# Kernel optimization log

Measured on AMD Instinct MI355X. Metric: run time of the kernel, lower is better.

Reference implementation:

```python
import jax, jax.numpy as jnp
import numpy as np

NUM_CLASSES = 21
THRESH = 0.5
NEG_POS = 3
VAR0, VAR1 = 0.1, 0.2  # SSD cfg['variance']
B, P, O = 32, 32768, 50


def point_form(boxes):
    # center form (cx,cy,w,h) -> corner form (xmin,ymin,xmax,ymax)
    return jnp.concatenate([boxes[:, :2] - boxes[:, 2:] / 2,
                            boxes[:, :2] + boxes[:, 2:] / 2], axis=1)


def jaccard(box_a, box_b):
    # box_a [A,4], box_b [B,4], corner form -> IoU [A,B]
    max_xy = jnp.minimum(box_a[:, None, 2:], box_b[None, :, 2:])
    min_xy = jnp.maximum(box_a[:, None, :2], box_b[None, :, :2])
    inter = jnp.prod(jnp.clip(max_xy - min_xy, 0.0, None), axis=2)
    area_a = jnp.prod(box_a[:, 2:] - box_a[:, :2], axis=1)[:, None]
    area_b = jnp.prod(box_b[:, 2:] - box_b[:, :2], axis=1)[None, :]
    return inter / (area_a + area_b - inter)


def encode(matched, priors):
    # matched corner form [P,4], priors center form [P,4]
    g_cxcy = ((matched[:, :2] + matched[:, 2:]) / 2 - priors[:, :2]) / (VAR0 * priors[:, 2:])
    g_wh = jnp.log((matched[:, 2:] - matched[:, :2]) / priors[:, 2:]) / VAR1
    return jnp.concatenate([g_cxcy, g_wh], axis=1)


def match_one(truths, labels, priors):
    # truths [O,4] corner, labels [O], priors [P,4] center
    overlaps = jaccard(truths, point_form(priors))          # [O,P]
    best_prior_idx = jnp.argmax(overlaps, axis=1)           # [O]
    best_truth_overlap = jnp.max(overlaps, axis=0)          # [P]
    best_truth_idx = jnp.argmax(overlaps, axis=0)           # [P]
    # ensure every gt matches its best prior
    best_truth_overlap = best_truth_overlap.at[best_prior_idx].set(2.0)
    best_truth_idx = best_truth_idx.at[best_prior_idx].set(jnp.arange(truths.shape[0]))
    matches = truths[best_truth_idx]                        # [P,4]
    conf = (labels[best_truth_idx] + 1.0).astype(jnp.int32)
    conf = jnp.where(best_truth_overlap < THRESH, 0, conf)
    return encode(matches, priors), conf


def setup_inputs() -> dict:
    key = jax.random.key(0)
    k1, k2, k3, k4, k5, k6 = jax.random.split(key, 6)
    loc_data = jax.random.normal(k1, (B, P, 4), dtype=jnp.float32)
    conf_data = jax.random.normal(k2, (B, P, NUM_CLASSES), dtype=jnp.float32)
    # priors in center form: centers in (0,1), sizes in (0.02, 0.5)
    cxy = jax.random.uniform(k3, (P, 2), dtype=jnp.float32)
    wh = jax.random.uniform(k4, (P, 2), dtype=jnp.float32, minval=0.02, maxval=0.5)
    priors = jnp.concatenate([cxy, wh], axis=1)
    # targets: valid corner-form boxes + label
    pts = jax.random.uniform(k5, (B, O, 2, 2), dtype=jnp.float32)
    xymin = pts.min(axis=2)
    xymax = jnp.maximum(pts.max(axis=2), xymin + 0.01)
    labels = jax.random.randint(k6, (B, O), 0, NUM_CLASSES - 1).astype(jnp.float32)
    targets = jnp.concatenate([xymin, xymax, labels[..., None]], axis=-1)
    return {"loc_data": loc_data, "conf_data": conf_data, "priors": priors, "targets": targets}


def reference(loc_data, conf_data, priors, targets):
    truths = targets[..., :4]
    labels = targets[..., 4]
    loc_t, conf_t = jax.vmap(match_one, in_axes=(0, 0, None))(truths, labels, priors)
    loc_t = jax.lax.stop_gradient(loc_t)
    conf_t = jax.lax.stop_gradient(conf_t)

    pos = conf_t > 0                                         # [B,P]
    # localization: smooth-L1, summed over positives
    diff = loc_data - loc_t
    ad = jnp.abs(diff)
    sl1 = jnp.where(ad < 1.0, 0.5 * diff * diff, ad - 0.5)
    loss_l = jnp.sum(sl1 * pos[..., None].astype(sl1.dtype))

    # per-prior softmax CE (logsumexp - true logit)
    lse = jax.nn.logsumexp(conf_data, axis=-1)               # [B,P]
    true_logit = jnp.take_along_axis(conf_data, conf_t[..., None], axis=-1)[..., 0]
    ce = lse - true_logit                                    # [B,P]

    # hard negative mining: rank negatives by CE (pos zeroed out)
    ce_mine = jnp.where(pos, 0.0, ce)
    loss_idx = jnp.argsort(-ce_mine, axis=1)
    idx_rank = jnp.argsort(loss_idx, axis=1)
    num_pos = jnp.sum(pos, axis=1, keepdims=True)            # [B,1]
    num_neg = jnp.clip(NEG_POS * num_pos, None, pos.shape[1] - 1)
    neg = idx_rank < num_neg

    sel = pos | neg
    loss_c = jnp.sum(jnp.where(sel, ce, 0.0))

    N = jnp.sum(num_pos).astype(loss_l.dtype)
    return loss_l / N, loss_c / N
```

## Files before the change

kernel.cpp:

```cpp
#include <hip/hip_runtime.h>
#include <math.h>

#define BB 32
#define PP 32768
#define OO 50
#define NT 25
#define NC 21
#define MPT 4

#define WBINLO (104 << 7)
#define WBINS  2048

typedef unsigned long long u64;
typedef unsigned int u32;
typedef unsigned char u8;

static constexpr u32 FORCED_HI = 0x40000000u;
static constexpr u32 HALF_BITS = 0x3F000000u;

static constexpr size_t OFF_WHC   = 0;
static constexpr size_t OFF_WHS   = OFF_WHC  + 4ull*BB*WBINS;
static constexpr size_t OFF_KEYS  = OFF_WHS  + 4ull*BB*WBINS;
static constexpr size_t OFF_NPOS  = OFF_KEYS + 8ull*BB*OO;
static constexpr size_t OFF_DACC  = OFF_NPOS + 128;
static constexpr size_t OFF_KEY2  = ((OFF_DACC + 8ull*3*BB + 127) & ~127ull);
static constexpr size_t ZERO_BYTES = OFF_KEY2 + 8ull*BB*PP;

__global__ __launch_bounds__(256) void zero_kernel(ulonglong2* __restrict__ dst, size_t n16) {
    size_t i = (size_t)blockIdx.x * 256 + threadIdx.x;
    if (i < n16) dst[i] = make_ulonglong2(0ull, 0ull);
}

static __device__ __forceinline__ float fast_div(float a, float b) {
    return a * __builtin_amdgcn_rcpf(b);
}

__global__ __launch_bounds__(256) void match_kernel(
    const float* __restrict__ priors, const float* __restrict__ targets,
    u64* __restrict__ key2, u64* __restrict__ keys)
{
#pragma clang fp contract(off)
    const int b = blockIdx.y;
    const int obase = blockIdx.z * NT;
    const int tid = threadIdx.x;
    const int lane = tid & 63, wid = tid >> 6;
    const int wbase = blockIdx.x * (256 * MPT) + wid * (64 * MPT);

    __shared__ float tr[NT * 5];
    __shared__ u64 wkeys[4][NT];
    if (tid < NT * 5) tr[tid] = targets[(size_t)b * OO * 5 + obase * 5 + tid];
    __syncthreads();

    float px1[MPT], py1[MPT], px2[MPT], py2[MPT], area_p[MPT];
#pragma unroll
    for (int s = 0; s < MPT; ++s) {
        int p = wbase + s * 64 + lane;
        float4 pr = *(const float4*)(priors + (size_t)p * 4);
        px1[s] = pr.x - pr.z * 0.5f; py1[s] = pr.y - pr.w * 0.5f;
        px2[s] = pr.x + pr.z * 0.5f; py2[s] = pr.y + pr.w * 0.5f;
        area_p[s] = (px2[s] - px1[s]) * (py2[s] - py1[s]);
    }

    float bestv[MPT]; int besto[MPT];
#pragma unroll
    for (int s = 0; s < MPT; ++s) { bestv[s] = -1.0f; besto[s] = 0; }

    for (int o = 0; o < NT; ++o) {
        float tx1 = tr[o*5+0], ty1 = tr[o*5+1], tx2 = tr[o*5+2], ty2 = tr[o*5+3];
        float area_t = (tx2 - tx1) * (ty2 - ty1);
        float iou[MPT];
#pragma unroll
        for (int s = 0; s < MPT; ++s) {
            float ix1 = fmaxf(tx1, px1[s]), iy1 = fmaxf(ty1, py1[s]);
            float ix2 = fminf(tx2, px2[s]), iy2 = fminf(ty2, py2[s]);
            float dx = fmaxf(ix2 - ix1, 0.0f), dy = fmaxf(iy2 - iy1, 0.0f);
            float inter = dx * dy;
            iou[s] = fast_div(inter, (area_t + area_p[s]) - inter);
            if (iou[s] > bestv[s]) { bestv[s] = iou[s]; besto[s] = o; }
        }
        float mv = fmaxf(fmaxf(iou[0], iou[1]), fmaxf(iou[2], iou[3]));
        for (int m = 1; m < 64; m <<= 1)
            mv = fmaxf(mv, __shfl_xor(mv, m, 64));
        u64 b0 = __ballot(iou[0] == mv);
        u64 b1 = __ballot(iou[1] == mv);
        u64 b2 = __ballot(iou[2] == mv);
        u64 b3 = __ballot(iou[3] == mv);
        if (lane == 0) {
            int s, l;
            if      (b0) { s = 0; l = __ffsll(b0) - 1; }
            else if (b1) { s = 1; l = __ffsll(b1) - 1; }
            else if (b2) { s = 2; l = __ffsll(b2) - 1; }
            else if (b3) { s = 3; l = __ffsll(b3) - 1; }
            else         { s = 0; l = 0; }
            u32 wp = (u32)(wbase + s * 64 + l);
            wkeys[wid][o] = ((u64)__float_as_uint(mv) << 32) | (u64)(0xFFFFFFFFu - wp);
        }
    }
#pragma unroll
    for (int s = 0; s < MPT; ++s) {
        int p = wbase + s * 64 + lane;
        u64 key = ((u64)__float_as_uint(bestv[s]) << 32)
                | (u64)(u32)(49 - (obase + besto[s]));
        atomicMax(&key2[(size_t)b * PP + p], key);
    }
    __syncthreads();
    if (tid < NT) {
        u64 k0 = wkeys[0][tid];
        for (int w = 1; w < 4; ++w) { u64 kw = wkeys[w][tid]; if (kw > k0) k0 = kw; }
        atomicMax(&keys[b * OO + obase + tid], k0);
    }
}

__global__ void override_kernel(const u64* __restrict__ keys, u64* __restrict__ key2) {
    const int b = blockIdx.x;
    const int o = threadIdx.x;
    if (o < OO) {
        u32 p = 0xFFFFFFFFu - (u32)(keys[b * OO + o] & 0xFFFFFFFFull);
        atomicMax(&key2[(size_t)b * PP + p],
                  ((u64)FORCED_HI << 32) | (u64)(u32)(64 + o));
    }
}

static __device__ __forceinline__ u32 top16bits(float v) {
    u32 u = __float_as_uint(v);
    return (v > 0.0f) ? u : 0u;
}

#define EL(k) ((((k) & 3) == 0) ? v[(k) >> 2].x : \
               (((k) & 3) == 1) ? v[(k) >> 2].y : \
               (((k) & 3) == 2) ? v[(k) >> 2].z : v[(k) >> 2].w)

__global__ __launch_bounds__(256) void score_kernel(
    const float* __restrict__ loc, const float* __restrict__ conf,
    const float* __restrict__ priors, const float* __restrict__ targets,
    const u64* __restrict__ key2,
    int* __restrict__ npos, double* __restrict__ dacc,
    u32* __restrict__ whc, float* __restrict__ whs)
{
    const int b = blockIdx.y;
    const int tid = threadIdx.x;
    const int p = blockIdx.x * 1024 + tid * 4;
    __shared__ float tr[OO * 5];
    __shared__ __align__(16) u32 hh[WBINS];
    __shared__ __align__(16) float hs[WBINS];
    if (tid < OO * 5) tr[tid] = targets[(size_t)b * OO * 5 + tid];
#pragma unroll
    for (int j = 0; j < WBINS / 256; ++j) { hh[j * 256 + tid] = 0; hs[j * 256 + tid] = 0.0f; }
    __syncthreads();

    ulonglong2 k01 = *(const ulonglong2*)(key2 + (size_t)b * PP + p);
    ulonglong2 k23 = *(const ulonglong2*)(key2 + (size_t)b * PP + p + 2);
    const u64 kk[4] = {k01.x, k01.y, k23.x, k23.y};

    const float4* cp = (const float4*)(conf + ((size_t)b * PP + p) * NC);
    float4 v[21];
    float cev[4];
    double l_l = 0.0, pce = 0.0; int np_ = 0;

#pragma unroll
    for (int r = 0; r < 4; ++r) {
        const int jlo = (r == 0) ? 0 : ((21 * (r - 1) + 20) / 4 + 1);
        const int jhi = (21 * r + 20) / 4;
#pragma unroll
        for (int j = jlo; j <= jhi; ++j) v[j] = cp[j];

        const u32 hi = (u32)(kk[r] >> 32);
        const u32 lo = (u32)kk[r];
        const bool forced = lo >= 64u;
        const int o = forced ? (int)(lo - 64u) : (int)(49u - lo);
        const bool pos = forced || hi >= HALF_BITS;
        const int conft = pos ? (int)(tr[o * 5 + 4] + 1.0f) : 0;

        float m = -1e30f;
#pragma unroll
        for (int c = 0; c < NC; ++c) m = fmaxf(m, EL(21 * r + c));
        float s = 0.0f, tl = 0.0f;
#pragma unroll
        for (int c = 0; c < NC; ++c) {
            float xx = EL(21 * r + c);
            s += expf(xx - m);
            if (c == conft) tl = xx;
        }
        float ce = (m + logf(s)) - tl;
        cev[r] = pos ? 0.0f : ce;

        if (pos) {
            np_ += 1; pce += (double)ce;
            float mx1 = tr[o*5+0], my1 = tr[o*5+1], mx2 = tr[o*5+2], my2 = tr[o*5+3];
            float4 pr = *(const float4*)(priors + (size_t)(p + r) * 4);
            float lt0 = ((mx1 + mx2) * 0.5f - pr.x) / (0.1f * pr.z);
            float lt1 = ((my1 + my2) * 0.5f - pr.y) / (0.1f * pr.w);
            float lt2 = logf((mx2 - mx1) / pr.z) / 0.2f;
            float lt3 = logf((my2 - my1) / pr.w) / 0.2f;
            float4 l4 = *(const float4*)(loc + ((size_t)b * PP + p + r) * 4);
            float lpv[4] = {l4.x, l4.y, l4.z, l4.w};
            float lt[4] = {lt0, lt1, lt2, lt3};
#pragma unroll
            for (int i2 = 0; i2 < 4; ++i2) {
                float d = lpv[i2] - lt[i2];
                float ad = fabsf(d);
                l_l += (double)(ad < 1.0f ? 0.5f * d * d : ad - 0.5f);
            }
        }
    }

#pragma unroll
    for (int r = 0; r < 4; ++r) {
        u32 t16 = top16bits(cev[r]) >> 16;
        if (t16 != 0) {
            int widx = ((int)t16 - WBINLO) >> 1;
            widx = widx < 0 ? 0 : (widx > WBINS - 1 ? WBINS - 1 : widx);
            atomicAdd(&hh[widx], 1u);
            atomicAdd(&hs[widx], cev[r]);
        }
    }
    __syncthreads();
#pragma unroll
    for (int j = 0; j < WBINS / 256; ++j) {
        u32 c = hh[j * 256 + tid];
        if (c) {
            atomicAdd(&whc[(size_t)b * WBINS + j * 256 + tid], c);
            atomicAdd(&whs[(size_t)b * WBINS + j * 256 + tid], hs[j * 256 + tid]);
        }
    }
    __syncthreads();
    double* rl = (double*)hh;
    double* rc = (double*)hs;
    int*    rn = (int*)(hh + 1024);
    rl[tid] = l_l; rc[tid] = pce; rn[tid] = np_;
    __syncthreads();
    for (int s2 = 128; s2 > 0; s2 >>= 1) {
        if (tid < s2) { rl[tid] += rl[tid+s2]; rc[tid] += rc[tid+s2]; rn[tid] += rn[tid+s2]; }
        __syncthreads();
    }
    if (tid == 0) {
        atomicAdd(&dacc[b], rl[0]);
        atomicAdd(&dacc[BB + b], rc[0]);
        atomicAdd(&npos[b], rn[0]);
    }
}

__global__ __launch_bounds__(256) void selwin_kernel(
    const u32* __restrict__ whc, const float* __restrict__ whs,
    const int* __restrict__ npos, double* __restrict__ dacc)
{
    const int b = blockIdx.x, tid = threadIdx.x;
    const int lane = tid & 63, wid = tid >> 6;
    int k = npos[b] * 3; if (k > PP - 1) k = PP - 1;
    if (k <= 0) return;
    const u32* hc = whc + (size_t)b * WBINS;
    const float* hsg = whs + (size_t)b * WBINS;

    __shared__ u32 ccnt_[WBINS / 256]; __shared__ float csum_[WBINS / 256];
    __shared__ u32 ct[256]; __shared__ float fs[256];
    __shared__ int s_cT; __shared__ u32 s_aboveC; __shared__ float s_aboveS;
    __shared__ u32 sT;

    for (int c = wid; c < WBINS / 256; c += 4) {
        u32 cnt = 0; float sm = 0.0f;
#pragma unroll
        for (int q = 0; q < 4; ++q) {
            int idx = c * 256 + q * 64 + lane;
            cnt += hc[idx];
            sm  += hsg[idx];
        }
        for (int m = 1; m < 64; m <<= 1) {
            cnt += __shfl_xor(cnt, m, 64);
            sm  += __shfl_xor(sm, m, 64);
        }
        if (lane == 0) { ccnt_[c] = cnt; csum_[c] = sm; }
    }
    if (tid == 0) sT = 0;
    __syncthreads();
    if (tid == 0) {
        u32 cum = 0; float scum = 0.0f; int cT = -1; u32 aboveC = 0; float aboveS = 0.0f;
        for (int c = WBINS / 256 - 1; c >= 0; --c) {
            if (cum + ccnt_[c] >= (u32)k) { cT = c; aboveC = cum; aboveS = scum; break; }
            cum += ccnt_[c]; scum += csum_[c];
        }
        s_cT = cT; s_aboveC = aboveC; s_aboveS = aboveS;
        if (cT < 0) dacc[2 * BB + b] = (double)scum;
    }
    __syncthreads();
    const int cT = s_cT;
    if (cT < 0) return;
    const u32 aboveC = s_aboveC; const float aboveS = s_aboveS;

    const u32 myc = hc[cT * 256 + tid];
    const float mys = hsg[cT * 256 + tid];
    ct[tid] = myc; fs[tid] = mys;
    __syncthreads();
    for (int off = 1; off < 256; off <<= 1) {
        u32 a1 = (tid + off < 256) ? ct[tid + off] : 0;
        float a2 = (tid + off < 256) ? fs[tid + off] : 0.0f;
        __syncthreads();
        ct[tid] += a1; fs[tid] += a2;
        __syncthreads();
    }
    if (aboveC + ct[tid] >= (u32)k) atomicMax(&sT, (u32)tid);
    __syncthreads();
    const int T = (int)sT;
    if (tid == T) {
        u32 aboveBinC = aboveC + ((T < 255) ? ct[T + 1] : 0);
        float aboveBinS = aboveS + ((T < 255) ? fs[T + 1] : 0.0f);
        int k2 = k - (int)aboveBinC;
        double avg = (double)mys / (double)myc;
        dacc[2 * BB + b] = (double)aboveBinS + (double)k2 * avg;
    }
}

__global__ void finalize_kernel(const int* __restrict__ npos,
                                const double* __restrict__ dacc, float* __restrict__ out) {
    if (threadIdx.x == 0 && blockIdx.x == 0) {
        double N = 0.0, ll = 0.0, lc = 0.0;
        for (int b = 0; b < BB; ++b) {
            N += (double)npos[b];
            ll += dacc[b];
            lc += dacc[BB + b] + dacc[2 * BB + b];
        }
        out[0] = (float)(ll / N);
        out[1] = (float)(lc / N);
    }
}

extern "C" void kernel_launch(void* const* d_in, const int* in_sizes, int n_in,
                              void* d_out, int out_size, void* d_ws, size_t ws_size,
                              hipStream_t stream) {
    const float* loc     = (const float*)d_in[0];
    const float* conf    = (const float*)d_in[1];
    const float* priors  = (const float*)d_in[2];
    const float* targets = (const float*)d_in[3];
    char* ws = (char*)d_ws;
    u32*    whc   = (u32*)   (ws + OFF_WHC);
    float*  whs   = (float*) (ws + OFF_WHS);
    u64*    keys  = (u64*)   (ws + OFF_KEYS);
    int*    npos  = (int*)   (ws + OFF_NPOS);
    double* dacc  = (double*)(ws + OFF_DACC);
    u64*    key2  = (u64*)   (ws + OFF_KEY2);
    float*  out   = (float*)d_out;

    const size_t n16 = ZERO_BYTES / 16;
    zero_kernel<<<(unsigned)((n16 + 255) / 256), 256, 0, stream>>>((ulonglong2*)ws, n16);
    match_kernel<<<dim3(PP / (256 * MPT), BB, 2), 256, 0, stream>>>(priors, targets, key2, keys);
    override_kernel<<<BB, 64, 0, stream>>>(keys, key2);
    score_kernel<<<dim3(PP / 1024, BB), 256, 0, stream>>>(loc, conf, priors, targets, key2, npos, dacc, whc, whs);
    selwin_kernel<<<BB, 256, 0, stream>>>(whc, whs, npos, dacc);
    finalize_kernel<<<1, 64, 0, stream>>>(npos, dacc, out);
}
```

Measured before the change: 98.97 us.

## Replace per-prior atomicMax with split key buffers and fold forced override into scoring

Each match_kernel half now writes plain stores into its own key2 slice instead of doing atomicMax into a shared slice. The score kernel loads both halves and takes the max. The key2 region no longer needs zeroing, which removes about 8 MB of memset traffic. The override kernel is also removed: the score kernel loads each image's 50 forced-match prior indices into shared memory and checks every prior against them. This saves a launch and the atomics, at the cost of double key2 reads in scoring and a 50-iteration compare loop per thread.

```diff
diff --git a/kernel.cpp b/kernel.cpp
--- a/kernel.cpp
+++ b/kernel.cpp
@@ -15,7 +15,6 @@
 typedef unsigned int u32;
 typedef unsigned char u8;
 
-static constexpr u32 FORCED_HI = 0x40000000u;
 static constexpr u32 HALF_BITS = 0x3F000000u;
 
 static constexpr size_t OFF_WHC   = 0;
@@ -23,8 +22,8 @@
 static constexpr size_t OFF_KEYS  = OFF_WHS  + 4ull*BB*WBINS;
 static constexpr size_t OFF_NPOS  = OFF_KEYS + 8ull*BB*OO;
 static constexpr size_t OFF_DACC  = OFF_NPOS + 128;
-static constexpr size_t OFF_KEY2  = ((OFF_DACC + 8ull*3*BB + 127) & ~127ull);
-static constexpr size_t ZERO_BYTES = OFF_KEY2 + 8ull*BB*PP;
+static constexpr size_t ZERO_BYTES = OFF_DACC + 8ull*3*BB;
+static constexpr size_t OFF_KEY2  = ((ZERO_BYTES + 127) & ~127ull);
 
 __global__ __launch_bounds__(256) void zero_kernel(ulonglong2* __restrict__ dst, size_t n16) {
     size_t i = (size_t)blockIdx.x * 256 + threadIdx.x;
@@ -41,7 +40,8 @@
 {
 #pragma clang fp contract(off)
     const int b = blockIdx.y;
-    const int obase = blockIdx.z * NT;
+    const int half = blockIdx.z;
+    const int obase = half * NT;
     const int tid = threadIdx.x;
     const int lane = tid & 63, wid = tid >> 6;
     const int wbase = blockIdx.x * (256 * MPT) + wid * (64 * MPT);
@@ -101,7 +101,7 @@
         int p = wbase + s * 64 + lane;
         u64 key = ((u64)__float_as_uint(bestv[s]) << 32)
                 | (u64)(u32)(49 - (obase + besto[s]));
-        atomicMax(&key2[(size_t)b * PP + p], key);
+        key2[((size_t)half * BB + b) * PP + p] = key;
     }
     __syncthreads();
     if (tid < NT) {
@@ -111,21 +111,13 @@
     }
 }
 
-__global__ void override_kernel(const u64* __restrict__ keys, u64* __restrict__ key2) {
-    const int b = blockIdx.x;
-    const int o = threadIdx.x;
-    if (o < OO) {
-        u32 p = 0xFFFFFFFFu - (u32)(keys[b * OO + o] & 0xFFFFFFFFull);
-        atomicMax(&key2[(size_t)b * PP + p],
-                  ((u64)FORCED_HI << 32) | (u64)(u32)(64 + o));
-    }
-}
-
 static __device__ __forceinline__ u32 top16bits(float v) {
     u32 u = __float_as_uint(v);
     return (v > 0.0f) ? u : 0u;
 }
 
+static __device__ __forceinline__ u64 umax64(u64 a, u64 b) { return a > b ? a : b; }
+
 #define EL(k) ((((k) & 3) == 0) ? v[(k) >> 2].x : \
                (((k) & 3) == 1) ? v[(k) >> 2].y : \
                (((k) & 3) == 2) ? v[(k) >> 2].z : v[(k) >> 2].w)
@@ -133,7 +125,7 @@
 __global__ __launch_bounds__(256) void score_kernel(
     const float* __restrict__ loc, const float* __restrict__ conf,
     const float* __restrict__ priors, const float* __restrict__ targets,
-    const u64* __restrict__ key2,
+    const u64* __restrict__ key2, const u64* __restrict__ keys,
     int* __restrict__ npos, double* __restrict__ dacc,
     u32* __restrict__ whc, float* __restrict__ whs)
 {
@@ -141,16 +133,28 @@
     const int tid = threadIdx.x;
     const int p = blockIdx.x * 1024 + tid * 4;
     __shared__ float tr[OO * 5];
+    __shared__ u32 fp[OO];
     __shared__ __align__(16) u32 hh[WBINS];
     __shared__ __align__(16) float hs[WBINS];
     if (tid < OO * 5) tr[tid] = targets[(size_t)b * OO * 5 + tid];
+    if (tid < OO) fp[tid] = 0xFFFFFFFFu - (u32)(keys[b * OO + tid] & 0xFFFFFFFFull);
 #pragma unroll
     for (int j = 0; j < WBINS / 256; ++j) { hh[j * 256 + tid] = 0; hs[j * 256 + tid] = 0.0f; }
     __syncthreads();
 
-    ulonglong2 k01 = *(const ulonglong2*)(key2 + (size_t)b * PP + p);
-    ulonglong2 k23 = *(const ulonglong2*)(key2 + (size_t)b * PP + p + 2);
-    const u64 kk[4] = {k01.x, k01.y, k23.x, k23.y};
+    ulonglong2 a01 = *(const ulonglong2*)(key2 + (size_t)b * PP + p);
+    ulonglong2 a23 = *(const ulonglong2*)(key2 + (size_t)b * PP + p + 2);
+    ulonglong2 c01 = *(const ulonglong2*)(key2 + ((size_t)BB + b) * PP + p);
+    ulonglong2 c23 = *(const ulonglong2*)(key2 + ((size_t)BB + b) * PP + p + 2);
+    const u64 kk[4] = {umax64(a01.x, c01.x), umax64(a01.y, c01.y),
+                       umax64(a23.x, c23.x), umax64(a23.y, c23.y)};
+
+    int fo[4] = {-1, -1, -1, -1};
+    for (int o = 0; o < OO; ++o) {
+        u32 fpo = fp[o];
+#pragma unroll
+        for (int r = 0; r < 4; ++r) if (fpo == (u32)(p + r)) fo[r] = o;
+    }
 
     const float4* cp = (const float4*)(conf + ((size_t)b * PP + p) * NC);
     float4 v[21];
@@ -166,8 +170,8 @@
 
         const u32 hi = (u32)(kk[r] >> 32);
         const u32 lo = (u32)kk[r];
-        const bool forced = lo >= 64u;
-        const int o = forced ? (int)(lo - 64u) : (int)(49u - lo);
+        const bool forced = fo[r] >= 0;
+        const int o = forced ? fo[r] : (int)(49u - lo);
         const bool pos = forced || hi >= HALF_BITS;
         const int conft = pos ? (int)(tr[o * 5 + 4] + 1.0f) : 0;
 
@@ -342,8 +346,7 @@
     const size_t n16 = ZERO_BYTES / 16;
     zero_kernel<<<(unsigned)((n16 + 255) / 256), 256, 0, stream>>>((ulonglong2*)ws, n16);
     match_kernel<<<dim3(PP / (256 * MPT), BB, 2), 256, 0, stream>>>(priors, targets, key2, keys);
-    override_kernel<<<BB, 64, 0, stream>>>(keys, key2);
-    score_kernel<<<dim3(PP / 1024, BB), 256, 0, stream>>>(loc, conf, priors, targets, key2, npos, dacc, whc, whs);
+    score_kernel<<<dim3(PP / 1024, BB), 256, 0, stream>>>(loc, conf, priors, targets, key2, keys, npos, dacc, whc, whs);
     selwin_kernel<<<BB, 256, 0, stream>>>(whc, whs, npos, dacc);
     finalize_kernel<<<1, 64, 0, stream>>>(npos, dacc, out);
 }
```

Result: no change. 98.62 us (-0.3%).
